# Optimization experiments

Hardware: AMD Instinct MI355X
Metric: run time of the kernel (lower is better)

The kernel has to match this reference:

```python
import jax, jax.numpy as jnp
import numpy as np

D = 1024
H = 16
HD = D // H  # 64
S = 2048
B = 1


def setup_inputs() -> dict:
    key = jax.random.key(0)
    ks = jax.random.split(key, 6)
    return {
        "GLO": jax.random.normal(ks[0], (B, S, D), dtype=jnp.float32),
        "LOC": jax.random.normal(ks[1], (B, S, D), dtype=jnp.float32),
        "W_q": jax.random.normal(ks[2], (H, D, HD), dtype=jnp.float32),
        "W_k": jax.random.normal(ks[3], (H, D, HD), dtype=jnp.float32),
        "W_v": jax.random.normal(ks[4], (H, D, HD), dtype=jnp.float32),
        "W_o": jax.random.normal(ks[5], (H * HD, D), dtype=jnp.float32),
    }


def _cross_attn(q_src, kv_src, W_q, W_k, W_v, W_o):
    # q_src: [B,Sq,D], kv_src: [B,Sk,D]
    b, sq, _ = q_src.shape
    Q = jnp.einsum('bsd,hde->bhse', q_src, W_q)   # [B,H,Sq,hd]
    K = jnp.einsum('bsd,hde->bhse', kv_src, W_k)  # [B,H,Sk,hd]
    V = jnp.einsum('bsd,hde->bhse', kv_src, W_v)  # [B,H,Sk,hd]
    scores = jnp.einsum('bhqe,bhke->bhqk', Q, K) / jnp.sqrt(jnp.float32(HD))
    weights = jax.nn.softmax(scores, axis=-1)
    out = jnp.einsum('bhqk,bhke->bhqe', weights, V)  # [B,H,Sq,hd]
    # Faithful to torch .view (raw memory reinterpretation, no head transpose)
    out = out.reshape(b, sq, H * HD)
    return out @ W_o  # [B,Sq,D]


def reference(GLO, LOC, W_q, W_k, W_v, W_o):
    GLO_prime = _cross_attn(GLO, LOC, W_q, W_k, W_v, W_o)
    LOC_prime = _cross_attn(LOC, GLO, W_q, W_k, W_v, W_o)
    return (GLO_prime, LOC_prime)
```

## Files before the change

kernel.cpp:

```cpp
#include <hip/hip_runtime.h>
#include <math.h>

#define S_LEN 2048
#define D_DIM 1024
#define NH 16
#define HD 64

typedef __attribute__((ext_vector_type(8))) short bf16x8;
typedef __attribute__((ext_vector_type(4))) float f32x4;

#define MFMA(a, b, c) __builtin_amdgcn_mfma_f32_16x16x32_bf16((a), (b), (c), 0, 0, 0)

__device__ __forceinline__ unsigned short f2bf(float x) {
    unsigned int u = __float_as_uint(x);
    u = (u + 0x7FFFu + ((u >> 16) & 1u)) >> 16;
    return (unsigned short)u;
}
__device__ __forceinline__ float bf2f(unsigned short b) {
    return __uint_as_float(((unsigned int)b) << 16);
}
__device__ __forceinline__ void gl_lds16(const void* g, void* l) {
    __builtin_amdgcn_global_load_lds((const __attribute__((address_space(1))) unsigned int*)g,
                                     (__attribute__((address_space(3))) unsigned int*)l, 16, 0, 0);
}

#if defined(__has_builtin)
#if __has_builtin(__builtin_amdgcn_cvt_pk_bf16_f32)
#define HAVE_CVT_PK_BF16 1
#endif
#endif
__device__ __forceinline__ unsigned pack_bf16(float a, float b) {
#ifdef HAVE_CVT_PK_BF16
    auto r = __builtin_amdgcn_cvt_pk_bf16_f32(a, b);
    unsigned u;
    __builtin_memcpy(&u, &r, 4);
    return u;
#else
    unsigned ua = __float_as_uint(a) + 0x8000u;
    unsigned ub = __float_as_uint(b) + 0x8000u;
    return __builtin_amdgcn_perm(ub, ua, 0x07060302u);
#endif
}


__global__ __launch_bounds__(256) void prep(const float* __restrict__ GLO,
                                            const float* __restrict__ LOC,
                                            const float* __restrict__ Wq,
                                            const float* __restrict__ Wk,
                                            const float* __restrict__ Wv,
                                            const float* __restrict__ Wo,
                                            unsigned short* __restrict__ Xh,
                                            unsigned short* __restrict__ Xl,
                                            unsigned short* __restrict__ Wqh,
                                            unsigned short* __restrict__ Wql,
                                            unsigned short* __restrict__ Wkh,
                                            unsigned short* __restrict__ Wkl,
                                            unsigned short* __restrict__ Wvt,
                                            unsigned short* __restrict__ Wot) {
    int idx = blockIdx.x * 256 + threadIdx.x;
    if (idx < (1 << 22)) {
        const float* src = (idx & (1 << 21)) ? LOC : GLO;
        float x = src[idx & ((1 << 21) - 1)];
        int r = idx >> 10;
        int k = idx & 1023;
        size_t t = (size_t)(r >> 7) * 131072 + (size_t)(k >> 6) * 8192 + (r & 127) * 64 +
                   ((((k >> 3) & 7) ^ (r & 7)) * 8) + (k & 7);
        unsigned short h = f2bf(x);
        Xh[t] = h;
        Xl[t] = f2bf(x - bf2f(h));
    } else {
        idx -= (1 << 22);
        int sec = idx >> 20;
        int i = idx & 0xFFFFF;
        if (sec < 3) {
            int e = i & 63;
            int d = (i >> 6) & 1023;
            int h = i >> 16;
            float wv = ((sec == 0) ? Wq : (sec == 1) ? Wk : Wv)[h * 65536 + d * 64 + e];
            size_t t = (size_t)h * 65536 + (size_t)(d >> 6) * 4096 + e * 64 +
                       ((((d >> 3) & 7) ^ (e & 7)) * 8) + (d & 7);
            if (sec == 0) {
                wv *= 0.18033688011112042f;
                unsigned short hi = f2bf(wv);
                Wqh[t] = hi;
                Wql[t] = f2bf(wv - bf2f(hi));
            } else if (sec == 1) {
                unsigned short hi = f2bf(wv);
                Wkh[t] = hi;
                Wkl[t] = f2bf(wv - bf2f(hi));
            } else {
                Wvt[t] = f2bf(wv);
            }
        } else {
            int n = i & 1023;
            int k = i >> 10;
            size_t t = (size_t)(n >> 6) * 65536 + (size_t)(k >> 6) * 4096 + (n & 63) * 64 +
                       ((((k >> 3) & 7) ^ (n & 7)) * 8) + (k & 7);
            Wot[t] = f2bf(Wo[k * 1024 + n]);
        }
    }
}

__global__ __launch_bounds__(256) void qkv_proj(const unsigned short* __restrict__ Xh,
                                                const unsigned short* __restrict__ Xl,
                                                const unsigned short* __restrict__ Wqh,
                                                const unsigned short* __restrict__ Wql,
                                                const unsigned short* __restrict__ Wkh,
                                                const unsigned short* __restrict__ Wkl,
                                                const unsigned short* __restrict__ Wvt,
                                                unsigned short* __restrict__ Qh,
                                                unsigned short* __restrict__ Ql,
                                                unsigned short* __restrict__ Kh,
                                                unsigned short* __restrict__ Kl,
                                                unsigned short* __restrict__ Vt) {
    __shared__ unsigned short lds[36864];
    const int bid = blockIdx.x;
    const int mblk = bid & 31;
    const int head = bid >> 5;
    const int tid = threadIdx.x;
    const int lane = tid & 63;
    const int w = tid >> 6;
    const int l15 = lane & 15, quad = lane >> 4;

    f32x4 aq[2][4] = {}, ak[2][4] = {}, av[2][4] = {};
    const size_t abase0 = (size_t)mblk * 131072;
    const size_t bbase0 = (size_t)head * 65536;

    for (int kb = 0; kb < 16; ++kb) {
        __syncthreads();
        {
            const size_t ab = abase0 + (size_t)kb * 8192;
            const size_t bb = bbase0 + (size_t)kb * 4096;
#pragma unroll
            for (int j = 0; j < 4; ++j) {
                int seg = j * 256 + tid;
                gl_lds16(Xh + ab + seg * 8, &lds[seg * 8]);
                gl_lds16(Xl + ab + seg * 8, &lds[8192 + seg * 8]);
            }
#pragma unroll
            for (int j = 0; j < 2; ++j) {
                int seg = j * 256 + tid;
                gl_lds16(Wqh + bb + seg * 8, &lds[16384 + seg * 8]);
                gl_lds16(Wql + bb + seg * 8, &lds[20480 + seg * 8]);
                gl_lds16(Wkh + bb + seg * 8, &lds[24576 + seg * 8]);
                gl_lds16(Wkl + bb + seg * 8, &lds[28672 + seg * 8]);
                gl_lds16(Wvt + bb + seg * 8, &lds[32768 + seg * 8]);
            }
        }
        __syncthreads();

#pragma unroll
        for (int ksub = 0; ksub < 2; ++ksub) {
            bf16x8 ah[2], al8[2];
#pragma unroll
            for (int mt = 0; mt < 2; ++mt) {
                int row = w * 32 + mt * 16 + l15;
                int g = (ksub * 4 + quad) ^ (row & 7);
                ah[mt] = *(const bf16x8*)&lds[row * 64 + g * 8];
                al8[mt] = *(const bf16x8*)&lds[8192 + row * 64 + g * 8];
            }
#pragma unroll
            for (int nt = 0; nt < 4; ++nt) {
                int col = nt * 16 + l15;
                int o = col * 64 + ((ksub * 4 + quad) ^ (col & 7)) * 8;
                bf16x8 bqh = *(const bf16x8*)&lds[16384 + o];
                bf16x8 bql = *(const bf16x8*)&lds[20480 + o];
                bf16x8 bkh = *(const bf16x8*)&lds[24576 + o];
                bf16x8 bkl = *(const bf16x8*)&lds[28672 + o];
                bf16x8 bv = *(const bf16x8*)&lds[32768 + o];
#pragma unroll
                for (int mt = 0; mt < 2; ++mt) {
                    f32x4 a = aq[mt][nt];
                    a = MFMA(ah[mt], bqh, a);
                    a = MFMA(ah[mt], bql, a);
                    a = MFMA(al8[mt], bqh, a);
                    aq[mt][nt] = a;
                    f32x4 b = ak[mt][nt];
                    b = MFMA(ah[mt], bkh, b);
                    b = MFMA(ah[mt], bkl, b);
                    b = MFMA(al8[mt], bkh, b);
                    ak[mt][nt] = b;
                    av[mt][nt] = MFMA(ah[mt], bv, av[mt][nt]);
                }
            }
        }
    }

#pragma unroll
    for (int mt = 0; mt < 2; ++mt) {
        const int rbase = mblk * 128 + w * 32 + mt * 16 + quad * 4;
#pragma unroll
        for (int nt = 0; nt < 4; ++nt) {
            const int col = head * 64 + nt * 16 + l15;
#pragma unroll
            for (int r = 0; r < 4; ++r) {
                size_t a = (size_t)(rbase + r) * D_DIM + col;
                float vq = aq[mt][nt][r];
                unsigned short hq = f2bf(vq);
                Qh[a] = hq;
                Ql[a] = f2bf(vq - bf2f(hq));
                float vk = ak[mt][nt][r];
                unsigned short hk = f2bf(vk);
                Kh[a] = hk;
                Kl[a] = f2bf(vk - bf2f(hk));
            }
            ushort4 vp;
            vp.x = f2bf(av[mt][nt][0]);
            vp.y = f2bf(av[mt][nt][1]);
            vp.z = f2bf(av[mt][nt][2]);
            vp.w = f2bf(av[mt][nt][3]);
            *(ushort4*)(Vt + (size_t)col * (2 * S_LEN) + rbase) = vp;
        }
    }
}

__global__ __launch_bounds__(256) void attn_kernel(const unsigned short* __restrict__ Qh_,
                                                   const unsigned short* __restrict__ Ql_,
                                                   const unsigned short* __restrict__ Kh_,
                                                   const unsigned short* __restrict__ Kl_,
                                                   const unsigned short* __restrict__ Vt_,
                                                   unsigned short* __restrict__ Oatt) {
    __shared__ unsigned short lds[28672];
    const int bid = blockIdx.x;
    const int qblk = bid & 15;
    const int head = (bid >> 4) & 15;
    const int dir = bid >> 8;
    const int src_q = dir, src_kv = 1 - dir;

    const int tid = threadIdx.x;
    const int lane = tid & 63;
    const int w = tid >> 6;
    const int l15 = lane & 15, quad = lane >> 4;
    const int q0w = qblk * 128 + w * 32;

    const unsigned short* KhB0 = Kh_ + (size_t)(src_kv * S_LEN) * D_DIM + head * 64;
    const unsigned short* KlB0 = Kl_ + (size_t)(src_kv * S_LEN) * D_DIM + head * 64;
    const unsigned short* Vtp = Vt_ + (size_t)(head * 64) * (2 * S_LEN) + src_kv * S_LEN;

    const int i0 = tid, i1 = 256 + tid;
    const int sr0 = i0 >> 3, sc0 = ((i0 & 7) ^ (sr0 & 7)) * 8;
    const int sr1 = i1 >> 3, sc1 = ((i1 & 7) ^ (sr1 & 7)) * 8;

    auto stage = [&](int k0, int boff) {
        const unsigned short* KhB = KhB0 + (size_t)k0 * D_DIM;
        const unsigned short* KlB = KlB0 + (size_t)k0 * D_DIM;
        const unsigned short* VB = Vtp + k0;
        gl_lds16(KhB + (size_t)sr0 * D_DIM + sc0, &lds[boff + i0 * 8]);
        gl_lds16(KhB + (size_t)sr1 * D_DIM + sc1, &lds[boff + i1 * 8]);
        gl_lds16(KlB + (size_t)sr0 * D_DIM + sc0, &lds[boff + 4096 + i0 * 8]);
        gl_lds16(KlB + (size_t)sr1 * D_DIM + sc1, &lds[boff + 4096 + i1 * 8]);
        gl_lds16(VB + (size_t)sr0 * (2 * S_LEN) + sc0, &lds[boff + 8192 + i0 * 8]);
        gl_lds16(VB + (size_t)sr1 * (2 * S_LEN) + sc1, &lds[boff + 8192 + i1 * 8]);
    };

    bf16x8 qh[2][2], ql[2][2];
#pragma unroll
    for (int mt = 0; mt < 2; ++mt) {
        const size_t qrow =
            (size_t)(src_q * S_LEN + q0w + mt * 16 + l15) * D_DIM + head * 64 + quad * 8;
#pragma unroll
        for (int c = 0; c < 2; ++c) {
            qh[mt][c] = *(const bf16x8*)(Qh_ + qrow + c * 32);
            ql[mt][c] = *(const bf16x8*)(Ql_ + qrow + c * 32);
        }
    }

    f32x4 o[2][4] = {};
    float mi[2] = {-1e30f, -1e30f};
    float lip[2] = {0.f, 0.f};
    unsigned short* Pw = lds + 24576 + w * 1024;

    auto chunk = [&](int kb) {
        f32x4 sa[2][4];
#pragma unroll
        for (int kt = 0; kt < 4; ++kt) {
            const int row = kt * 16 + l15;
            const int s0 = (quad ^ (row & 7)) * 8;
            const int s1 = ((4 + quad) ^ (row & 7)) * 8;
            bf16x8 kh0 = *(const bf16x8*)&lds[kb + row * 64 + s0];
            bf16x8 kh1 = *(const bf16x8*)&lds[kb + row * 64 + s1];
            bf16x8 kl0 = *(const bf16x8*)&lds[kb + 4096 + row * 64 + s0];
            bf16x8 kl1 = *(const bf16x8*)&lds[kb + 4096 + row * 64 + s1];
#pragma unroll
            for (int mt = 0; mt < 2; ++mt) {
                f32x4 a = {};
                a = MFMA(kh0, qh[mt][0], a);
                a = MFMA(kh1, qh[mt][1], a);
                a = MFMA(kl0, qh[mt][0], a);
                a = MFMA(kl1, qh[mt][1], a);
                a = MFMA(kh0, ql[mt][0], a);
                a = MFMA(kh1, ql[mt][1], a);
                sa[mt][kt] = a;
            }
        }

#pragma unroll
        for (int mt = 0; mt < 2; ++mt) {
            f32x4 t4 = __builtin_elementwise_max(__builtin_elementwise_max(sa[mt][0], sa[mt][1]),
                                                 __builtin_elementwise_max(sa[mt][2], sa[mt][3]));
            float tm = fmaxf(fmaxf(t4[0], t4[1]), fmaxf(t4[2], t4[3]));
            tm = fmaxf(tm, __shfl_xor(tm, 16, 64));
            tm = fmaxf(tm, __shfl_xor(tm, 32, 64));
            if (__ballot(tm > mi[mt])) {
                float mn = fmaxf(mi[mt], tm);
                float al = exp2f(mi[mt] - mn);
                mi[mt] = mn;
                lip[mt] *= al;
                const f32x4 alv = {al, al, al, al};
#pragma unroll
                for (int et = 0; et < 4; ++et) o[mt][et] *= alv;
            }
            const float mn = mi[mt];
            const f32x4 mnv = {mn, mn, mn, mn};
            f32x4 rs4 = {};
#pragma unroll
            for (int kt = 0; kt < 4; ++kt) {
                f32x4 p = sa[mt][kt] - mnv;
#pragma unroll
                for (int r = 0; r < 4; ++r) p[r] = exp2f(p[r]);
                rs4 += p;
                uint2 pk;
                pk.x = pack_bf16(p[0], p[1]);
                pk.y = pack_bf16(p[2], p[3]);
                int g = (kt * 2 + (quad >> 1)) ^ (l15 & 7);
                *(uint2*)&Pw[l15 * 64 + g * 8 + (quad & 1) * 4] = pk;
            }
            lip[mt] += (rs4[0] + rs4[1]) + (rs4[2] + rs4[3]);

#pragma unroll
            for (int c = 0; c < 2; ++c) {
                bf16x8 pf = *(const bf16x8*)&Pw[l15 * 64 + (((c * 4 + quad) ^ (l15 & 7)) * 8)];
#pragma unroll
                for (int et = 0; et < 4; ++et) {
                    const int row = et * 16 + l15;
                    const int sl = ((c * 4 + quad) ^ (row & 7)) * 8;
                    bf16x8 vf = *(const bf16x8*)&lds[kb + 8192 + row * 64 + sl];
                    o[mt][et] = MFMA(vf, pf, o[mt][et]);
                }
            }
        }
    };

    stage(0, 0);
#pragma unroll 1
    for (int kd = 0; kd < 32; kd += 2) {
        __syncthreads();
        if (kd + 1 < 32) stage((kd + 1) * 64, 12288);
        chunk(0);
        __syncthreads();
        if (kd + 2 < 32) stage((kd + 2) * 64, 0);
        chunk(12288);
    }

    const size_t obase = (size_t)(dir * 16 + head) * 131072 + (size_t)l15 * 8192;
#pragma unroll
    for (int mt = 0; mt < 2; ++mt) {
        float lq = lip[mt];
        lq += __shfl_xor(lq, 16, 64);
        lq += __shfl_xor(lq, 32, 64);
        float rl = __builtin_amdgcn_rcpf(lq);
        const int rowit = qblk * 8 + w * 2 + mt;
#pragma unroll
        for (int et = 0; et < 4; ++et) {
            int g = ((et * 2 + (quad >> 1)) ^ (rowit & 7)) & 7;
            ushort4 pk;
            pk.x = f2bf(o[mt][et][0] * rl);
            pk.y = f2bf(o[mt][et][1] * rl);
            pk.z = f2bf(o[mt][et][2] * rl);
            pk.w = f2bf(o[mt][et][3] * rl);
            *(ushort4*)(Oatt + obase + (size_t)rowit * 64 + g * 8 + (quad & 1) * 4) = pk;
        }
    }
}

__global__ __launch_bounds__(256) void oproj(const unsigned short* __restrict__ Oatt,
                                             const unsigned short* __restrict__ Wot,
                                             float* __restrict__ out) {
    __shared__ unsigned short lds[24576];
    const int bid = blockIdx.x;
    const int nblk = bid & 15;
    const int mblk = bid >> 4;
    const int tid = threadIdx.x;
    const int lane = tid & 63, w = tid >> 6, l15 = lane & 15, quad = lane >> 4;

    f32x4 acc[2][4] = {};
    const size_t abase = (size_t)mblk * 131072;
    const size_t bbase = (size_t)nblk * 65536;

    auto ostage = [&](int kb, int boff) {
#pragma unroll
        for (int j = 0; j < 4; ++j) {
            int seg = j * 256 + tid;
            gl_lds16(Oatt + abase + (size_t)kb * 8192 + seg * 8, &lds[boff + seg * 8]);
        }
#pragma unroll
        for (int j = 0; j < 2; ++j) {
            int seg = j * 256 + tid;
            gl_lds16(Wot + bbase + (size_t)kb * 4096 + seg * 8, &lds[boff + 8192 + seg * 8]);
        }
    };

    auto compute = [&](int boff) {
#pragma unroll
        for (int ksub = 0; ksub < 2; ++ksub) {
            bf16x8 a[2];
#pragma unroll
            for (int mt = 0; mt < 2; ++mt) {
                int row = w * 32 + mt * 16 + l15;
                a[mt] =
                    *(const bf16x8*)&lds[boff + row * 64 + (((ksub * 4 + quad) ^ (row & 7)) * 8)];
            }
#pragma unroll
            for (int nt = 0; nt < 4; ++nt) {
                int col = nt * 16 + l15;
                bf16x8 b = *(const bf16x8*)&lds[boff + 8192 + col * 64 +
                                                (((ksub * 4 + quad) ^ (col & 7)) * 8)];
#pragma unroll
                for (int mt = 0; mt < 2; ++mt) acc[mt][nt] = MFMA(a[mt], b, acc[mt][nt]);
            }
        }
    };

    ostage(0, 0);
#pragma unroll 1
    for (int kb = 0; kb < 16; kb += 2) {
        __syncthreads();
        if (kb + 1 < 16) ostage(kb + 1, 12288);
        compute(0);
        __syncthreads();
        if (kb + 2 < 16) ostage(kb + 2, 0);
        compute(12288);
    }

#pragma unroll
    for (int mt = 0; mt < 2; ++mt) {
        const int rbase = mblk * 128 + w * 32 + mt * 16 + quad * 4;
#pragma unroll
        for (int nt = 0; nt < 4; ++nt)
#pragma unroll
            for (int r = 0; r < 4; ++r)
                out[(size_t)(rbase + r) * D_DIM + nblk * 64 + nt * 16 + l15] = acc[mt][nt][r];
    }
}

extern "C" void kernel_launch(void* const* d_in, const int* in_sizes, int n_in, void* d_out,
                              int out_size, void* d_ws, size_t ws_size, hipStream_t stream) {
    const float* GLO = (const float*)d_in[0];
    const float* LOC = (const float*)d_in[1];
    const float* Wq = (const float*)d_in[2];
    const float* Wk = (const float*)d_in[3];
    const float* Wv = (const float*)d_in[4];
    const float* Wo = (const float*)d_in[5];
    float* out = (float*)d_out;

    unsigned short* ws = (unsigned short*)d_ws;
    unsigned short* Xh = ws + 0;
    unsigned short* Xl = ws + 4194304;
    unsigned short* Wqh = ws + 8388608;
    unsigned short* Wql = ws + 9437184;
    unsigned short* Wkh = ws + 10485760;
    unsigned short* Wkl = ws + 11534336;
    unsigned short* Wvt = ws + 12582912;
    unsigned short* Wot = ws + 13631488;
    unsigned short* Qh = ws + 14680064;
    unsigned short* Ql = ws + 18874368;
    unsigned short* Kh = ws + 23068672;
    unsigned short* Kl = ws + 27262976;
    unsigned short* Vt = ws + 31457280;
    unsigned short* Oatt = ws + 35651584;

    prep<<<32768, 256, 0, stream>>>(GLO, LOC, Wq, Wk, Wv, Wo, Xh, Xl, Wqh, Wql, Wkh, Wkl, Wvt, Wot);
    qkv_proj<<<512, 256, 0, stream>>>(Xh, Xl, Wqh, Wql, Wkh, Wkl, Wvt, Qh, Ql, Kh, Kl, Vt);
    attn_kernel<<<512, 256, 0, stream>>>(Qh, Ql, Kh, Kl, Vt, Oatt);
    oproj<<<512, 256, 0, stream>>>(Oatt, Wot, out);
}
```

Before: 274.1 us.

## Pack hi/lo bf16 splits together and double-buffer QKV projection LDS staging

The prep kernel now interleaves the hi and lo bf16 halves of X, Wq and Wk into a single packed, swizzled layout with 32-wide k chunks. It also repacks Wv to match. The QKV projection kernel uses two LDS buffers, so the global-to-LDS load of the next k chunk is issued while the current chunk is computed. This replaces the previous load, sync, compute pattern and is meant to hide global memory latency. The cost is a smaller chunk per sync, twice as many chunks, and more complex swizzle indexing.

```diff
diff --git a/kernel.cpp b/kernel.cpp
--- a/kernel.cpp
+++ b/kernel.cpp
@@ -49,13 +49,10 @@
                                             const float* __restrict__ Wk,
                                             const float* __restrict__ Wv,
                                             const float* __restrict__ Wo,
-                                            unsigned short* __restrict__ Xh,
-                                            unsigned short* __restrict__ Xl,
-                                            unsigned short* __restrict__ Wqh,
-                                            unsigned short* __restrict__ Wql,
-                                            unsigned short* __restrict__ Wkh,
-                                            unsigned short* __restrict__ Wkl,
-                                            unsigned short* __restrict__ Wvt,
+                                            unsigned short* __restrict__ Xpk,
+                                            unsigned short* __restrict__ Wqpk,
+                                            unsigned short* __restrict__ Wkpk,
+                                            unsigned short* __restrict__ Wvpk,
                                             unsigned short* __restrict__ Wot) {
     int idx = blockIdx.x * 256 + threadIdx.x;
     if (idx < (1 << 22)) {
@@ -63,11 +60,11 @@
         float x = src[idx & ((1 << 21) - 1)];
         int r = idx >> 10;
         int k = idx & 1023;
-        size_t t = (size_t)(r >> 7) * 131072 + (size_t)(k >> 6) * 8192 + (r & 127) * 64 +
-                   ((((k >> 3) & 7) ^ (r & 7)) * 8) + (k & 7);
+        size_t tb = (size_t)(r >> 7) * 262144 + (size_t)(k >> 5) * 8192 + (r & 127) * 64 + (k & 7);
+        int kg = (k >> 3) & 3, r7 = r & 7;
         unsigned short h = f2bf(x);
-        Xh[t] = h;
-        Xl[t] = f2bf(x - bf2f(h));
+        Xpk[tb + (size_t)((kg ^ r7)) * 8] = h;
+        Xpk[tb + (size_t)(((4 + kg) ^ r7)) * 8] = f2bf(x - bf2f(h));
     } else {
         idx -= (1 << 22);
         int sec = idx >> 20;
@@ -75,21 +72,27 @@
         if (sec < 3) {
             int e = i & 63;
             int d = (i >> 6) & 1023;
-            int h = i >> 16;
-            float wv = ((sec == 0) ? Wq : (sec == 1) ? Wk : Wv)[h * 65536 + d * 64 + e];
-            size_t t = (size_t)h * 65536 + (size_t)(d >> 6) * 4096 + e * 64 +
-                       ((((d >> 3) & 7) ^ (e & 7)) * 8) + (d & 7);
+            int hh = i >> 16;
+            float wv = ((sec == 0) ? Wq : (sec == 1) ? Wk : Wv)[hh * 65536 + d * 64 + e];
             if (sec == 0) {
                 wv *= 0.18033688011112042f;
+                size_t tb =
+                    (size_t)hh * 131072 + (size_t)(d >> 5) * 4096 + e * 64 + (d & 7);
+                int kg = (d >> 3) & 3, e7 = e & 7;
                 unsigned short hi = f2bf(wv);
-                Wqh[t] = hi;
-                Wql[t] = f2bf(wv - bf2f(hi));
+                Wqpk[tb + (size_t)((kg ^ e7)) * 8] = hi;
+                Wqpk[tb + (size_t)(((4 + kg) ^ e7)) * 8] = f2bf(wv - bf2f(hi));
             } else if (sec == 1) {
+                size_t tb =
+                    (size_t)hh * 131072 + (size_t)(d >> 5) * 4096 + e * 64 + (d & 7);
+                int kg = (d >> 3) & 3, e7 = e & 7;
                 unsigned short hi = f2bf(wv);
-                Wkh[t] = hi;
-                Wkl[t] = f2bf(wv - bf2f(hi));
+                Wkpk[tb + (size_t)((kg ^ e7)) * 8] = hi;
+                Wkpk[tb + (size_t)(((4 + kg) ^ e7)) * 8] = f2bf(wv - bf2f(hi));
             } else {
-                Wvt[t] = f2bf(wv);
+                size_t t = (size_t)hh * 65536 + (size_t)(d >> 5) * 2048 + e * 32 +
+                           (size_t)((((d >> 3) & 3) ^ (e & 3))) * 8 + (d & 7);
+                Wvpk[t] = f2bf(wv);
             }
         } else {
             int n = i & 1023;
@@ -101,13 +104,10 @@
     }
 }
 
-__global__ __launch_bounds__(256) void qkv_proj(const unsigned short* __restrict__ Xh,
-                                                const unsigned short* __restrict__ Xl,
-                                                const unsigned short* __restrict__ Wqh,
-                                                const unsigned short* __restrict__ Wql,
-                                                const unsigned short* __restrict__ Wkh,
-                                                const unsigned short* __restrict__ Wkl,
-                                                const unsigned short* __restrict__ Wvt,
+__global__ __launch_bounds__(256) void qkv_proj(const unsigned short* __restrict__ Xpk,
+                                                const unsigned short* __restrict__ Wqpk,
+                                                const unsigned short* __restrict__ Wkpk,
+                                                const unsigned short* __restrict__ Wvpk,
                                                 unsigned short* __restrict__ Qh,
                                                 unsigned short* __restrict__ Ql,
                                                 unsigned short* __restrict__ Kh,
@@ -123,67 +123,70 @@
     const int l15 = lane & 15, quad = lane >> 4;
 
     f32x4 aq[2][4] = {}, ak[2][4] = {}, av[2][4] = {};
-    const size_t abase0 = (size_t)mblk * 131072;
-    const size_t bbase0 = (size_t)head * 65536;
-
-    for (int kb = 0; kb < 16; ++kb) {
-        __syncthreads();
-        {
-            const size_t ab = abase0 + (size_t)kb * 8192;
-            const size_t bb = bbase0 + (size_t)kb * 4096;
-#pragma unroll
-            for (int j = 0; j < 4; ++j) {
-                int seg = j * 256 + tid;
-                gl_lds16(Xh + ab + seg * 8, &lds[seg * 8]);
-                gl_lds16(Xl + ab + seg * 8, &lds[8192 + seg * 8]);
-            }
-#pragma unroll
-            for (int j = 0; j < 2; ++j) {
-                int seg = j * 256 + tid;
-                gl_lds16(Wqh + bb + seg * 8, &lds[16384 + seg * 8]);
-                gl_lds16(Wql + bb + seg * 8, &lds[20480 + seg * 8]);
-                gl_lds16(Wkh + bb + seg * 8, &lds[24576 + seg * 8]);
-                gl_lds16(Wkl + bb + seg * 8, &lds[28672 + seg * 8]);
-                gl_lds16(Wvt + bb + seg * 8, &lds[32768 + seg * 8]);
-            }
-        }
-        __syncthreads();
-
-#pragma unroll
-        for (int ksub = 0; ksub < 2; ++ksub) {
-            bf16x8 ah[2], al8[2];
+    const size_t xb = (size_t)mblk * 262144;
+    const size_t qb = (size_t)head * 131072;
+    const size_t kbw = (size_t)head * 131072;
+    const size_t vbw = (size_t)head * 65536;
+
+    auto stage = [&](int kc, int boff) {
+#pragma unroll
+        for (int j = 0; j < 4; ++j) {
+            int u = j * 256 + tid;
+            gl_lds16(Xpk + xb + (size_t)kc * 8192 + u * 8, &lds[boff + u * 8]);
+        }
+#pragma unroll
+        for (int j = 0; j < 2; ++j) {
+            int u = j * 256 + tid;
+            gl_lds16(Wqpk + qb + (size_t)kc * 4096 + u * 8, &lds[boff + 8192 + u * 8]);
+            gl_lds16(Wkpk + kbw + (size_t)kc * 4096 + u * 8, &lds[boff + 12288 + u * 8]);
+        }
+        gl_lds16(Wvpk + vbw + (size_t)kc * 2048 + tid * 8, &lds[boff + 16384 + tid * 8]);
+    };
+
+    auto compute = [&](int boff) {
+        bf16x8 ah[2], al8[2];
+#pragma unroll
+        for (int mt = 0; mt < 2; ++mt) {
+            int row = w * 32 + mt * 16 + l15;
+            ah[mt] = *(const bf16x8*)&lds[boff + row * 64 + ((quad ^ (row & 7))) * 8];
+            al8[mt] = *(const bf16x8*)&lds[boff + row * 64 + (((4 + quad) ^ (row & 7))) * 8];
+        }
+#pragma unroll
+        for (int nt = 0; nt < 4; ++nt) {
+            int col = nt * 16 + l15;
+            int g_h = (quad ^ (col & 7)) * 8;
+            int g_l = ((4 + quad) ^ (col & 7)) * 8;
+            bf16x8 bqh = *(const bf16x8*)&lds[boff + 8192 + col * 64 + g_h];
+            bf16x8 bql = *(const bf16x8*)&lds[boff + 8192 + col * 64 + g_l];
+            bf16x8 bkh = *(const bf16x8*)&lds[boff + 12288 + col * 64 + g_h];
+            bf16x8 bkl = *(const bf16x8*)&lds[boff + 12288 + col * 64 + g_l];
+            bf16x8 bv = *(const bf16x8*)&lds[boff + 16384 + col * 32 + ((quad ^ (col & 3))) * 8];
 #pragma unroll
             for (int mt = 0; mt < 2; ++mt) {
-                int row = w * 32 + mt * 16 + l15;
-                int g = (ksub * 4 + quad) ^ (row & 7);
-                ah[mt] = *(const bf16x8*)&lds[row * 64 + g * 8];
-                al8[mt] = *(const bf16x8*)&lds[8192 + row * 64 + g * 8];
-            }
-#pragma unroll
-            for (int nt = 0; nt < 4; ++nt) {
-                int col = nt * 16 + l15;
-                int o = col * 64 + ((ksub * 4 + quad) ^ (col & 7)) * 8;
-                bf16x8 bqh = *(const bf16x8*)&lds[16384 + o];
-                bf16x8 bql = *(const bf16x8*)&lds[20480 + o];
-                bf16x8 bkh = *(const bf16x8*)&lds[24576 + o];
-                bf16x8 bkl = *(const bf16x8*)&lds[28672 + o];
-                bf16x8 bv = *(const bf16x8*)&lds[32768 + o];
-#pragma unroll
-                for (int mt = 0; mt < 2; ++mt) {
-                    f32x4 a = aq[mt][nt];
-                    a = MFMA(ah[mt], bqh, a);
-                    a = MFMA(ah[mt], bql, a);
-                    a = MFMA(al8[mt], bqh, a);
-                    aq[mt][nt] = a;
-                    f32x4 b = ak[mt][nt];
-                    b = MFMA(ah[mt], bkh, b);
-                    b = MFMA(ah[mt], bkl, b);
-                    b = MFMA(al8[mt], bkh, b);
-                    ak[mt][nt] = b;
-                    av[mt][nt] = MFMA(ah[mt], bv, av[mt][nt]);
-                }
-            }
-        }
+                f32x4 a = aq[mt][nt];
+                a = MFMA(ah[mt], bqh, a);
+                a = MFMA(ah[mt], bql, a);
+                a = MFMA(al8[mt], bqh, a);
+                aq[mt][nt] = a;
+                f32x4 b = ak[mt][nt];
+                b = MFMA(ah[mt], bkh, b);
+                b = MFMA(ah[mt], bkl, b);
+                b = MFMA(al8[mt], bkh, b);
+                ak[mt][nt] = b;
+                av[mt][nt] = MFMA(ah[mt], bv, av[mt][nt]);
+            }
+        }
+    };
+
+    stage(0, 0);
+#pragma unroll 1
+    for (int kc = 0; kc < 32; kc += 2) {
+        __syncthreads();
+        if (kc + 1 < 32) stage(kc + 1, 18432);
+        compute(0);
+        __syncthreads();
+        if (kc + 2 < 32) stage(kc + 2, 0);
+        compute(18432);
     }
 
 #pragma unroll
@@ -454,13 +457,10 @@
     float* out = (float*)d_out;
 
     unsigned short* ws = (unsigned short*)d_ws;
-    unsigned short* Xh = ws + 0;
-    unsigned short* Xl = ws + 4194304;
-    unsigned short* Wqh = ws + 8388608;
-    unsigned short* Wql = ws + 9437184;
-    unsigned short* Wkh = ws + 10485760;
-    unsigned short* Wkl = ws + 11534336;
-    unsigned short* Wvt = ws + 12582912;
+    unsigned short* Xpk = ws + 0;
+    unsigned short* Wqpk = ws + 8388608;
+    unsigned short* Wkpk = ws + 10485760;
+    unsigned short* Wvpk = ws + 12582912;
     unsigned short* Wot = ws + 13631488;
     unsigned short* Qh = ws + 14680064;
     unsigned short* Ql = ws + 18874368;
@@ -469,8 +469,8 @@
     unsigned short* Vt = ws + 31457280;
     unsigned short* Oatt = ws + 35651584;
 
-    prep<<<32768, 256, 0, stream>>>(GLO, LOC, Wq, Wk, Wv, Wo, Xh, Xl, Wqh, Wql, Wkh, Wkl, Wvt, Wot);
-    qkv_proj<<<512, 256, 0, stream>>>(Xh, Xl, Wqh, Wql, Wkh, Wkl, Wvt, Qh, Ql, Kh, Kl, Vt);
+    prep<<<32768, 256, 0, stream>>>(GLO, LOC, Wq, Wk, Wv, Wo, Xpk, Wqpk, Wkpk, Wvpk, Wot);
+    qkv_proj<<<512, 256, 0, stream>>>(Xpk, Wqpk, Wkpk, Wvpk, Qh, Ql, Kh, Kl, Vt);
     attn_kernel<<<512, 256, 0, stream>>>(Qh, Ql, Kh, Kl, Vt, Oatt);
     oproj<<<512, 256, 0, stream>>>(Oatt, Wot, out);
 }
```

Result: slower. 299.0 us (+9.1%).
